# Performance work log

Hardware: AMD Instinct MI355X
Metric: run time of the kernel (lower is better)

The kernel has to match this reference:

```python
import jax, jax.numpy as jnp
import numpy as np

B, L, D, H = 8, 1024, 1024, 16
DK = D // H  # 64
LN_EPS = 1e-5
L2_EPS = 1e-12


def _l2norm(x):
    # torch F.normalize(dim=-1): x / max(||x||_2, eps)
    n = jnp.sqrt(jnp.sum(x * x, axis=-1, keepdims=True))
    return x / jnp.maximum(n, L2_EPS)


def _layernorm(x, gamma, beta):
    mu = jnp.mean(x, axis=-1, keepdims=True)
    var = jnp.mean((x - mu) ** 2, axis=-1, keepdims=True)
    return (x - mu) * jax.lax.rsqrt(var + LN_EPS) * gamma + beta


def setup_inputs() -> dict:
    key = jax.random.key(0)
    ks = jax.random.split(key, 12)
    s = 0.02
    inp = {
        "Q": jax.random.normal(ks[0], (B, L, D), jnp.float32),
        "ctx": jax.random.normal(ks[1], (B, L, D), jnp.float32),
        "attn_mask": jnp.triu(jnp.ones((L, L), bool), 1),  # True = masked (causal)
        # weights stored [in, out] (= torch weight.T) so y = x @ W + b
        "W_q": jax.random.normal(ks[2], (D, D), jnp.float32) * s,
        "b_q": jnp.zeros((D,), jnp.float32),
        "W_k": jax.random.normal(ks[3], (D, D), jnp.float32) * s,
        "b_k": jnp.zeros((D,), jnp.float32),
        "W_v": jax.random.normal(ks[4], (D, D), jnp.float32) * s,
        "b_v": jnp.zeros((D,), jnp.float32),
        "bilinear": jax.random.normal(ks[5], (DK, DK), jnp.float32),
        "ln_gamma": jnp.ones((DK,), jnp.float32),
        "ln_beta": jnp.zeros((DK,), jnp.float32),
        "scale": jnp.asarray(DK ** -0.5, jnp.float32),
        "bias_scale": jnp.asarray(0.1, jnp.float32),
        "W_o": jax.random.normal(ks[6], (D, D), jnp.float32) * s,
        "b_o": jnp.zeros((D,), jnp.float32),
    }
    return inp


def reference(Q, ctx, attn_mask, W_q, b_q, W_k, b_k, W_v, b_v, bilinear,
              ln_gamma, ln_beta, scale, bias_scale, W_o, b_o):
    def split_heads(x):  # [B,L,D] -> [B,H,L,DK]
        return x.reshape(B, L, H, DK).transpose(0, 2, 1, 3)

    q = split_heads(Q @ W_q + b_q)
    k = split_heads(Q @ W_k + b_k)  # self-attention: K = V = Q
    v = split_heads(Q @ W_v + b_v)

    scores = jnp.einsum("bhqd,bhkd->bhqk", q, k) * scale  # [B,H,L,L]
    scores = jnp.where(attn_mask, -jnp.inf, scores)
    attn = jax.nn.softmax(scores, axis=-1)

    # post-softmax bilinear bias: LayerNorm -> bilinear matmul -> L2-normalize
    c = _layernorm(split_heads(ctx), ln_gamma, ln_beta)  # [B,H,L,DK]
    bias = jnp.einsum("bhqe,bhke->bhqk", c @ bilinear, c)  # [B,H,L,L]
    attn = attn + _l2norm(bias) * bias_scale
    attn = _l2norm(attn)

    out = jnp.einsum("bhqk,bhkd->bhqd", attn, v)  # [B,H,L,DK]
    out = out.transpose(0, 2, 1, 3).reshape(B, L, D)
    out = out @ W_o + b_o
    return out
```

## Files before the change

kernel.cpp:

```cpp
#include <hip/hip_runtime.h>


typedef __bf16 bf16;
typedef __bf16 bf16x8 __attribute__((ext_vector_type(8)));
typedef __bf16 bf16x4 __attribute__((ext_vector_type(4)));
typedef float  f32x4  __attribute__((ext_vector_type(4)));

#define DEV static __device__ __forceinline__

DEV f32x4 mfma16(bf16x8 a, bf16x8 b, f32x4 c) {
  return __builtin_amdgcn_mfma_f32_16x16x32_bf16(a, b, c, 0, 0, 0);
}

DEV void async16(void* lds, const void* g) {
  auto* d = reinterpret_cast<__attribute__((address_space(3))) unsigned int*>(
      (unsigned long long)lds);
  auto* s = reinterpret_cast<const __attribute__((address_space(1))) unsigned int*>(
      (unsigned long long)g);
  __builtin_amdgcn_global_load_lds(s, d, 16, 0, 0);
}


__global__ __launch_bounds__(256) void k_cvt(const float* __restrict__ in,
                                             bf16* __restrict__ out, int n4) {
  int i = blockIdx.x * 256 + threadIdx.x;
  if (i >= n4) return;
  f32x4 v = ((const f32x4*)in)[i];
  bf16x4 o = {(bf16)v.x, (bf16)v.y, (bf16)v.z, (bf16)v.w};
  ((bf16x4*)out)[i] = o;
}

__global__ __launch_bounds__(256) void k_transpose_w(const float* __restrict__ in,
                                                     bf16* __restrict__ out) {
  __shared__ float t[64][65];
  const int k0 = blockIdx.x * 64, n0 = blockIdx.y * 64;
  for (int e = threadIdx.x; e < 4096; e += 256) {
    int r = e >> 6, c = e & 63;
    t[r][c] = in[(size_t)(k0 + r) * 1024 + n0 + c];
  }
  __syncthreads();
  for (int e = threadIdx.x; e < 4096; e += 256) {
    int r = e >> 6, c = e & 63;
    out[(size_t)(n0 + r) * 1024 + k0 + c] = (bf16)t[c][r];
  }
}

__global__ __launch_bounds__(256, 4) void k_ln_bilinear(
    const float* __restrict__ ctx, const float* __restrict__ bil,
    const float* __restrict__ gam, const float* __restrict__ bet,
    bf16* __restrict__ c_out, bf16* __restrict__ cb_out) {
  const int w = threadIdx.x >> 6, lane = threadIdx.x & 63;
  float bilreg[64];
#pragma unroll
  for (int e = 0; e < 64; ++e) bilreg[e] = bil[e * 64 + lane];
  const float gm = gam[lane], bt = bet[lane];
  const int wid = blockIdx.x * 4 + w;
  for (int it = 0; it < 16; ++it) {
    const int row = wid * 16 + it;
    const int h = row & 15, bl = row >> 4;
    const float x = ctx[(size_t)row * 64 + lane];
    float s1 = x, s2 = x * x;
#pragma unroll
    for (int mm = 32; mm >= 1; mm >>= 1) {
      s1 += __shfl_xor(s1, mm);
      s2 += __shfl_xor(s2, mm);
    }
    const float mu = s1 * 0.015625f;
    const float var = s2 * 0.015625f - mu * mu;
    const float cv = (x - mu) * rsqrtf(var + 1e-5f) * gm + bt;
    float a0 = 0.f, a1 = 0.f, a2 = 0.f, a3 = 0.f;
#pragma unroll
    for (int e = 0; e < 64; e += 4) {
      a0 += __int_as_float(__builtin_amdgcn_readlane(__float_as_int(cv), e + 0)) * bilreg[e + 0];
      a1 += __int_as_float(__builtin_amdgcn_readlane(__float_as_int(cv), e + 1)) * bilreg[e + 1];
      a2 += __int_as_float(__builtin_amdgcn_readlane(__float_as_int(cv), e + 2)) * bilreg[e + 2];
      a3 += __int_as_float(__builtin_amdgcn_readlane(__float_as_int(cv), e + 3)) * bilreg[e + 3];
    }
    const float acc = (a0 + a1) + (a2 + a3);
    const size_t o =
        ((size_t)((bl >> 10) * 16 + h) * 1024 + (bl & 1023)) * 64 + lane;
    c_out[o] = (bf16)cv;
    cb_out[o] = (bf16)acc;
  }
}


struct GemmPtrs {
  const bf16* Bt[3];
  bf16* ob[3];
  const float* bias[3];
};

__global__ __launch_bounds__(256) void k_gemm(const bf16* __restrict__ A,
                                              GemmPtrs p,
                                              float* __restrict__ outf,
                                              int mode) {
  __shared__ __align__(16) bf16 lds[2][2][4096];
  const int tid = threadIdx.x;
  const int bm = blockIdx.x, bn = blockIdx.y, z = blockIdx.z;
  const int w = tid >> 6, lane = tid & 63, g = lane >> 4, x = lane & 15;
  const int wr = w >> 1, wc = w & 1;
  const bf16* Bt = p.Bt[z];
  const float* bias = p.bias[z];
  bf16* ob = p.ob[z];

  f32x4 acc[4][4];
#pragma unroll
  for (int mt = 0; mt < 4; ++mt)
#pragma unroll
    for (int nt = 0; nt < 4; ++nt) acc[mt][nt] = f32x4{0.f, 0.f, 0.f, 0.f};

  const bf16* Ab = A + (size_t)bm * 128 * 1024;
  const bf16* Bb = Bt + (size_t)bn * 128 * 1024;

  auto stage = [&](int buf, int t) {
#pragma unroll
    for (int i = 0; i < 2; ++i) {
      int ch = i * 256 + tid;
      int r = ch >> 2, s = ch & 3;
      int sg = (s ^ ((r >> 1) & 3)) * 8;
      async16(&lds[buf][0][ch * 8], Ab + (size_t)r * 1024 + t * 32 + sg);
      async16(&lds[buf][1][ch * 8], Bb + (size_t)r * 1024 + t * 32 + sg);
    }
  };

  stage(0, 0);
  const int sa = (g ^ ((x >> 1) & 3)) * 8;
  for (int kt = 0; kt < 32; ++kt) {
    __syncthreads();
    if (kt + 1 < 32) stage((kt + 1) & 1, kt + 1);
    const bf16* la = lds[kt & 1][0];
    const bf16* lb = lds[kt & 1][1];
    bf16x8 af[4], bfr[4];
#pragma unroll
    for (int mt = 0; mt < 4; ++mt)
      af[mt] = *(const bf16x8*)(la + (wr * 64 + mt * 16 + x) * 32 + sa);
#pragma unroll
    for (int nt = 0; nt < 4; ++nt)
      bfr[nt] = *(const bf16x8*)(lb + (wc * 64 + nt * 16 + x) * 32 + sa);
#pragma unroll
    for (int mt = 0; mt < 4; ++mt)
#pragma unroll
      for (int nt = 0; nt < 4; ++nt)
        acc[mt][nt] = mfma16(af[mt], bfr[nt], acc[mt][nt]);
  }

  const int ibase = bm * 128 + wr * 64;
  const int jbase = bn * 128 + wc * 64;
  float bias4[4];
#pragma unroll
  for (int nt = 0; nt < 4; ++nt) bias4[nt] = bias[jbase + nt * 16 + x];

  if (mode < 3) {
    if (z == 2) {
#pragma unroll
      for (int mt = 0; mt < 4; ++mt)
#pragma unroll
        for (int nt = 0; nt < 4; ++nt) {
          const int jj = jbase + nt * 16 + x;
          const int hh = jj >> 6, dk = jj & 63;
          const int i0 = ibase + mt * 16 + 4 * g;
          const int bb = i0 >> 10, l0 = i0 & 1023;
          bf16x4 v4 = {(bf16)(acc[mt][nt][0] + bias4[nt]),
                       (bf16)(acc[mt][nt][1] + bias4[nt]),
                       (bf16)(acc[mt][nt][2] + bias4[nt]),
                       (bf16)(acc[mt][nt][3] + bias4[nt])};
          *(bf16x4*)&ob[((size_t)(bb * 16 + hh) * 64 + dk) * 1024 + l0] = v4;
        }
    } else {
#pragma unroll
      for (int mt = 0; mt < 4; ++mt)
#pragma unroll
        for (int nt = 0; nt < 4; ++nt) {
          const int jj = jbase + nt * 16 + x;
          const int hh = jj >> 6, dk = jj & 63;
#pragma unroll
          for (int j = 0; j < 4; ++j) {
            const int i = ibase + mt * 16 + 4 * g + j;
            const int bb = i >> 10, l = i & 1023;
            ob[(((size_t)bb * 16 + hh) * 1024 + l) * 64 + dk] =
                (bf16)(acc[mt][nt][j] + bias4[nt]);
          }
        }
    }
  } else {
#pragma unroll
    for (int mt = 0; mt < 4; ++mt)
#pragma unroll
      for (int nt = 0; nt < 4; ++nt) {
        const int jj = jbase + nt * 16 + x;
#pragma unroll
        for (int j = 0; j < 4; ++j) {
          const int i = ibase + mt * 16 + 4 * g + j;
          outf[(size_t)i * 1024 + jj] = acc[mt][nt][j] + bias4[nt];
        }
      }
  }
}

__global__ __launch_bounds__(256, 4) void k_attn(
    const bf16* __restrict__ qg, const bf16* __restrict__ kg,
    const bf16* __restrict__ vTg, const bf16* __restrict__ cg,
    const bf16* __restrict__ cbg, bf16* __restrict__ ao,
    const float* __restrict__ scale_p, const float* __restrict__ bsp) {
  __shared__ __align__(16) bf16 kl[2][2048];
  __shared__ __align__(16) bf16 cl[2][2048];
  __shared__ __align__(16) bf16 vl[2][64][36];
  __shared__ __align__(16) bf16 pe[4][640];
  __shared__ __align__(16) bf16 pb[4][640];

  const float scl = scale_p[0];
  const float bsc = bsp[0];
  const int tid = threadIdx.x, w = tid >> 6, lane = tid & 63;
  const int g = lane >> 4, x = lane & 15;
  const int id = blockIdx.x;
  const int xcd = id & 7, sid = id >> 3;
  const int bh = xcd * 16 + (sid >> 4);
  const int qt = sid & 15;
  const int qrow0 = qt * 64 + w * 16;

  const bf16* qrow = qg + ((size_t)bh * 1024 + qrow0 + x) * 64;
  const bf16* cbrow = cbg + ((size_t)bh * 1024 + qrow0 + x) * 64;
  const bf16x8 qf0 = *(const bf16x8*)(qrow + 8 * g);
  const bf16x8 qf1 = *(const bf16x8*)(qrow + 32 + 8 * g);
  const bf16x8 cbf0 = *(const bf16x8*)(cbrow + 8 * g);
  const bf16x8 cbf1 = *(const bf16x8*)(cbrow + 32 + 8 * g);

  f32x4 acc1[4], acc2[4];
#pragma unroll
  for (int i = 0; i < 4; ++i) {
    acc1[i] = f32x4{0.f, 0.f, 0.f, 0.f};
    acc2[i] = f32x4{0.f, 0.f, 0.f, 0.f};
  }
  float Zs = 0.f, E2 = 0.f, Cc = 0.f, B2 = 0.f;

  const bf16* kbh = kg + (size_t)bh * 65536;
  const bf16* cbh = cg + (size_t)bh * 65536;
  const bf16* vbh = vTg + (size_t)bh * 65536;
  const int nK = 2 * qt + 2;

  auto stageKC = [&](int buf, int t) {
    const int r = tid >> 3, s = tid & 7;
    const int sg = (s ^ (r & 7)) * 8;
    if (t < nK)
      async16(&kl[buf][tid * 8], kbh + (size_t)(t * 32 + r) * 64 + sg);
    async16(&cl[buf][tid * 8], cbh + (size_t)(t * 32 + r) * 64 + sg);
  };
  bf16x8 vreg;
  auto loadV = [&](int t) {
    const int r = tid >> 2, s = tid & 3;
    vreg = *(const bf16x8*)(vbh + (size_t)r * 1024 + t * 32 + s * 8);
  };
  auto writeV = [&](int buf) {
    const int r = tid >> 2, s = tid & 3;
    *(bf16x8*)&vl[buf][r][(s ^ (r & 3)) * 8] = vreg;
  };

  stageKC(0, 0);
  loadV(0);
  writeV(0);
  for (int t = 0; t < 32; ++t) {
    __syncthreads();
    if (t + 1 < 32) {
      stageKC((t + 1) & 1, t + 1);
      loadV(t + 1);
    }
    const bf16* klb = kl[t & 1];
    const bf16* clb = cl[t & 1];
    const int tileK = t * 32;
    const bool hv = tileK <= qrow0 + 15;
    float sv[8], bv[8];
#pragma unroll
    for (int sub = 0; sub < 2; ++sub) {
      const int rloc = sub * 16 + x;
      const int so0 = (g ^ (rloc & 7)) * 8;
      const int so1 = ((4 + g) ^ (rloc & 7)) * 8;
      const bf16* cr = clb + rloc * 64;
      f32x4 bacc = f32x4{0.f, 0.f, 0.f, 0.f};
      bacc = mfma16(*(const bf16x8*)(cr + so0), cbf0, bacc);
      bacc = mfma16(*(const bf16x8*)(cr + so1), cbf1, bacc);
      const int k16 = tileK + sub * 16;
      const bool av = k16 <= qrow0 + 15;
      const bool full = (k16 + 15) <= qrow0;
      f32x4 sacc = f32x4{0.f, 0.f, 0.f, 0.f};
      if (av) {
        const bf16* kr = klb + rloc * 64;
        sacc = mfma16(*(const bf16x8*)(kr + so0), qf0, sacc);
        sacc = mfma16(*(const bf16x8*)(kr + so1), qf1, sacc);
      }
      const int q = qrow0 + x;
#pragma unroll
      for (int j = 0; j < 4; ++j) {
        bv[sub * 4 + j] = bacc[j];
        B2 += bacc[j] * bacc[j];
        const int kk = k16 + 4 * g + j;
        sv[sub * 4 + j] =
            full ? sacc[j] * scl
                 : ((av && kk <= q) ? sacc[j] * scl : -1e30f);
      }
    }
    if (hv) {
      float ev[8];
#pragma unroll
      for (int jj = 0; jj < 8; ++jj) {
        const float e = __expf(sv[jj]);
        ev[jj] = e;
        Zs += e; E2 += e * e; Cc += e * bv[jj];
      }
      bf16x4 e0 = {(bf16)ev[0], (bf16)ev[1], (bf16)ev[2], (bf16)ev[3]};
      bf16x4 e1 = {(bf16)ev[4], (bf16)ev[5], (bf16)ev[6], (bf16)ev[7]};
      *(bf16x4*)&pe[w][x * 40 + 4 * g] = e0;
      *(bf16x4*)&pe[w][x * 40 + 16 + 4 * g] = e1;
    }
    bf16x4 b0 = {(bf16)bv[0], (bf16)bv[1], (bf16)bv[2], (bf16)bv[3]};
    bf16x4 b1 = {(bf16)bv[4], (bf16)bv[5], (bf16)bv[6], (bf16)bv[7]};
    *(bf16x4*)&pb[w][x * 40 + 4 * g] = b0;
    *(bf16x4*)&pb[w][x * 40 + 16 + 4 * g] = b1;
    const bf16x8 pbf = *(const bf16x8*)&pb[w][x * 40 + 8 * g];
#pragma unroll
    for (int nt = 0; nt < 4; ++nt) {
      const int dr = nt * 16 + x;
      const bf16x8 vf = *(const bf16x8*)&vl[t & 1][dr][(g ^ (dr & 3)) * 8];
      acc2[nt] = mfma16(pbf, vf, acc2[nt]);
    }
    if (hv) {
      const bf16x8 pef = *(const bf16x8*)&pe[w][x * 40 + 8 * g];
#pragma unroll
      for (int nt = 0; nt < 4; ++nt) {
        const int dr = nt * 16 + x;
        const bf16x8 vf = *(const bf16x8*)&vl[t & 1][dr][(g ^ (dr & 3)) * 8];
        acc1[nt] = mfma16(pef, vf, acc1[nt]);
      }
    }
    if (t + 1 < 32) writeV((t + 1) & 1);
  }

  Zs += __shfl_xor(Zs, 16); Zs += __shfl_xor(Zs, 32);
  E2 += __shfl_xor(E2, 16); E2 += __shfl_xor(E2, 32);
  Cc += __shfl_xor(Cc, 16); Cc += __shfl_xor(Cc, 32);
  B2 += __shfl_xor(B2, 16); B2 += __shfl_xor(B2, 32);
  const float bnorm = fmaxf(sqrtf(B2), 1e-12f);
  const float invZ = 1.0f / Zs;
  const float n2 = E2 * invZ * invZ + 2.0f * bsc * Cc * invZ / bnorm +
                   bsc * bsc * B2 / (bnorm * bnorm);
  const float inv_an = 1.0f / fmaxf(sqrtf(n2), 1e-12f);
  const float cA = invZ * inv_an;
  const float cB = bsc / bnorm * inv_an;
  const int b_ = bh >> 4, h_ = bh & 15;
#pragma unroll
  for (int j = 0; j < 4; ++j) {
    const int src = (lane & 48) | (4 * g + j);
    const float cAj = __shfl(cA, src);
    const float cBj = __shfl(cB, src);
    const int qr = qrow0 + 4 * g + j;
#pragma unroll
    for (int nt = 0; nt < 4; ++nt) {
      const float o = cAj * acc1[nt][j] + cBj * acc2[nt][j];
      ao[(size_t)(b_ * 1024 + qr) * 1024 + h_ * 64 + nt * 16 + x] = (bf16)o;
    }
  }
}


extern "C" void kernel_launch(void* const* d_in, const int* in_sizes, int n_in,
                              void* d_out, int out_size, void* d_ws,
                              size_t ws_size, hipStream_t stream) {
  const float* Q   = (const float*)d_in[0];
  const float* ctx = (const float*)d_in[1];
  const float* Wq  = (const float*)d_in[3];
  const float* bq  = (const float*)d_in[4];
  const float* Wk  = (const float*)d_in[5];
  const float* bk  = (const float*)d_in[6];
  const float* Wv  = (const float*)d_in[7];
  const float* bvp = (const float*)d_in[8];
  const float* bil = (const float*)d_in[9];
  const float* gam = (const float*)d_in[10];
  const float* bet = (const float*)d_in[11];
  const float* scl = (const float*)d_in[12];
  const float* bsc = (const float*)d_in[13];
  const float* Wo  = (const float*)d_in[14];
  const float* bo  = (const float*)d_in[15];
  float* out = (float*)d_out;
  char* ws = (char*)d_ws;
  const size_t MB = 1ull << 20;

  bf16* Qb  = (bf16*)(ws + 0);
  bf16* Wtq = (bf16*)(ws + 16 * MB);
  bf16* Wtk = (bf16*)(ws + 18 * MB);
  bf16* Wtv = (bf16*)(ws + 20 * MB);
  bf16* Wto = (bf16*)(ws + 22 * MB);
  bf16* qb  = (bf16*)(ws + 24 * MB);
  bf16* kb  = (bf16*)(ws + 40 * MB);
  bf16* vT  = (bf16*)(ws + 72 * MB);
  bf16* cN  = (bf16*)(ws + 88 * MB);
  bf16* cbN = (bf16*)(ws + 104 * MB);
  bf16* ao  = Qb;

  k_cvt<<<8192, 256, 0, stream>>>(Q, Qb, 2097152);
  k_transpose_w<<<dim3(16, 16), 256, 0, stream>>>(Wq, Wtq);
  k_transpose_w<<<dim3(16, 16), 256, 0, stream>>>(Wk, Wtk);
  k_transpose_w<<<dim3(16, 16), 256, 0, stream>>>(Wv, Wtv);
  k_transpose_w<<<dim3(16, 16), 256, 0, stream>>>(Wo, Wto);
  k_ln_bilinear<<<2048, 256, 0, stream>>>(ctx, bil, gam, bet, cN, cbN);

  GemmPtrs p1{{Wtq, Wtk, Wtv}, {qb, kb, vT}, {bq, bk, bvp}};
  k_gemm<<<dim3(64, 8, 3), 256, 0, stream>>>(Qb, p1, nullptr, 0);

  k_attn<<<2048, 256, 0, stream>>>(qb, kb, vT, cN, cbN, ao, scl, bsc);

  GemmPtrs p2{{Wto, Wto, Wto}, {nullptr, nullptr, nullptr}, {bo, bo, bo}};
  k_gemm<<<dim3(64, 8, 1), 256, 0, stream>>>(ao, p2, out, 3);

  (void)in_sizes; (void)n_in; (void)out_size; (void)ws_size;
}
```

Baseline: 411.6 us.

## Factor bilinear bias through per-head Gram matrices and skip masked key tiles

The bilinear-bias term over all keys is low-rank, so it is rewritten algebraically. Per-head matrices M = Vᵀ·C and G = Cᵀ·C are precomputed in a new kernel, so the bias contribution to the output and its squared norm become small 64x64 products per query row. The cross term between softmax weights and bias is obtained by accumulating P·C alongside P·V. This lets the attention loop stop at the causal boundary instead of scanning all 1024 keys, roughly halving the work. It costs an extra transpose of C, a small Gram kernel, and some extra bf16 rounding in the norm computation.

Measured after the change: 422.6 us. +2.7%, slower.

```diff
diff --git a/kernel.cpp b/kernel.cpp
--- a/kernel.cpp
+++ b/kernel.cpp
@@ -42,6 +42,23 @@
   for (int e = threadIdx.x; e < 4096; e += 256) {
     int r = e >> 6, c = e & 63;
     out[(size_t)(n0 + r) * 1024 + k0 + c] = (bf16)t[c][r];
+  }
+}
+
+__global__ __launch_bounds__(256) void k_transpose_c(const bf16* __restrict__ in,
+                                                     bf16* __restrict__ out) {
+  __shared__ bf16 t[64][65];
+  const int bh = blockIdx.y, k0 = blockIdx.x * 64;
+  const bf16* src = in + (size_t)bh * 65536;
+  bf16* dst = out + (size_t)bh * 65536;
+  for (int e = threadIdx.x; e < 4096; e += 256) {
+    int r = e >> 6, c = e & 63;
+    t[r][c] = src[(size_t)(k0 + r) * 64 + c];
+  }
+  __syncthreads();
+  for (int e = threadIdx.x; e < 4096; e += 256) {
+    int r = e >> 6, c = e & 63;
+    dst[(size_t)r * 1024 + k0 + c] = t[c][r];
   }
 }
 
@@ -82,6 +99,35 @@
     c_out[o] = (bf16)cv;
     cb_out[o] = (bf16)acc;
   }
+}
+
+__global__ __launch_bounds__(256) void k_mg(const bf16* __restrict__ vT,
+                                            const bf16* __restrict__ cT,
+                                            bf16* __restrict__ mg) {
+  const int which = blockIdx.x, bh = blockIdx.y;
+  const int w = threadIdx.x >> 6, lane = threadIdx.x & 63;
+  const int g = lane >> 4, x = lane & 15;
+  const bf16* A = (which ? cT : vT) + (size_t)bh * 65536;
+  const bf16* Bm = cT + (size_t)bh * 65536;
+  f32x4 acc[4];
+#pragma unroll
+  for (int nt = 0; nt < 4; ++nt) acc[nt] = f32x4{0.f, 0.f, 0.f, 0.f};
+  const bf16* arow = A + (size_t)(w * 16 + x) * 1024 + 8 * g;
+  for (int k = 0; k < 32; ++k) {
+    const bf16x8 af = *(const bf16x8*)(arow + k * 32);
+#pragma unroll
+    for (int nt = 0; nt < 4; ++nt) {
+      const bf16x8 bf = *(const bf16x8*)(Bm + (size_t)(nt * 16 + x) * 1024 +
+                                         k * 32 + 8 * g);
+      acc[nt] = mfma16(af, bf, acc[nt]);
+    }
+  }
+  bf16* out = mg + (size_t)bh * 8192 + which * 4096;
+#pragma unroll
+  for (int nt = 0; nt < 4; ++nt)
+#pragma unroll
+    for (int j = 0; j < 4; ++j)
+      out[(w * 16 + 4 * g + j) * 64 + nt * 16 + x] = (bf16)acc[nt][j];
 }
 
 
@@ -200,14 +246,14 @@
 
 __global__ __launch_bounds__(256, 4) void k_attn(
     const bf16* __restrict__ qg, const bf16* __restrict__ kg,
-    const bf16* __restrict__ vTg, const bf16* __restrict__ cg,
-    const bf16* __restrict__ cbg, bf16* __restrict__ ao,
+    const bf16* __restrict__ vTg, const bf16* __restrict__ cTg,
+    const bf16* __restrict__ cbg, const bf16* __restrict__ mg,
+    bf16* __restrict__ ao,
     const float* __restrict__ scale_p, const float* __restrict__ bsp) {
   __shared__ __align__(16) bf16 kl[2][2048];
-  __shared__ __align__(16) bf16 cl[2][2048];
+  __shared__ __align__(16) bf16 ctl[2][64][36];
   __shared__ __align__(16) bf16 vl[2][64][36];
   __shared__ __align__(16) bf16 pe[4][640];
-  __shared__ __align__(16) bf16 pb[4][640];
 
   const float scl = scale_p[0];
   const float bsc = bsp[0];
@@ -226,136 +272,175 @@
   const bf16x8 cbf0 = *(const bf16x8*)(cbrow + 8 * g);
   const bf16x8 cbf1 = *(const bf16x8*)(cbrow + 32 + 8 * g);
 
-  f32x4 acc1[4], acc2[4];
+  f32x4 acc1[4], acc3[4];
 #pragma unroll
   for (int i = 0; i < 4; ++i) {
     acc1[i] = f32x4{0.f, 0.f, 0.f, 0.f};
-    acc2[i] = f32x4{0.f, 0.f, 0.f, 0.f};
-  }
-  float Zs = 0.f, E2 = 0.f, Cc = 0.f, B2 = 0.f;
+    acc3[i] = f32x4{0.f, 0.f, 0.f, 0.f};
+  }
+  float Zs = 0.f, E2 = 0.f;
 
   const bf16* kbh = kg + (size_t)bh * 65536;
-  const bf16* cbh = cg + (size_t)bh * 65536;
+  const bf16* ctbh = cTg + (size_t)bh * 65536;
   const bf16* vbh = vTg + (size_t)bh * 65536;
   const int nK = 2 * qt + 2;
 
-  auto stageKC = [&](int buf, int t) {
+  auto stageK = [&](int buf, int t) {
     const int r = tid >> 3, s = tid & 7;
     const int sg = (s ^ (r & 7)) * 8;
-    if (t < nK)
-      async16(&kl[buf][tid * 8], kbh + (size_t)(t * 32 + r) * 64 + sg);
-    async16(&cl[buf][tid * 8], cbh + (size_t)(t * 32 + r) * 64 + sg);
+    async16(&kl[buf][tid * 8], kbh + (size_t)(t * 32 + r) * 64 + sg);
   };
-  bf16x8 vreg;
-  auto loadV = [&](int t) {
+  bf16x8 vreg, creg;
+  auto loadCV = [&](int t) {
     const int r = tid >> 2, s = tid & 3;
     vreg = *(const bf16x8*)(vbh + (size_t)r * 1024 + t * 32 + s * 8);
+    creg = *(const bf16x8*)(ctbh + (size_t)r * 1024 + t * 32 + s * 8);
   };
-  auto writeV = [&](int buf) {
+  auto writeCV = [&](int buf) {
     const int r = tid >> 2, s = tid & 3;
     *(bf16x8*)&vl[buf][r][(s ^ (r & 3)) * 8] = vreg;
+    *(bf16x8*)&ctl[buf][r][(s ^ (r & 3)) * 8] = creg;
   };
 
-  stageKC(0, 0);
-  loadV(0);
-  writeV(0);
-  for (int t = 0; t < 32; ++t) {
+  stageK(0, 0);
+  loadCV(0);
+  writeCV(0);
+  for (int t = 0; t < nK; ++t) {
     __syncthreads();
-    if (t + 1 < 32) {
-      stageKC((t + 1) & 1, t + 1);
-      loadV(t + 1);
+    if (t + 1 < nK) {
+      stageK((t + 1) & 1, t + 1);
+      loadCV(t + 1);
     }
     const bf16* klb = kl[t & 1];
-    const bf16* clb = cl[t & 1];
     const int tileK = t * 32;
     const bool hv = tileK <= qrow0 + 15;
-    float sv[8], bv[8];
-#pragma unroll
-    for (int sub = 0; sub < 2; ++sub) {
-      const int rloc = sub * 16 + x;
-      const int so0 = (g ^ (rloc & 7)) * 8;
-      const int so1 = ((4 + g) ^ (rloc & 7)) * 8;
-      const bf16* cr = clb + rloc * 64;
-      f32x4 bacc = f32x4{0.f, 0.f, 0.f, 0.f};
-      bacc = mfma16(*(const bf16x8*)(cr + so0), cbf0, bacc);
-      bacc = mfma16(*(const bf16x8*)(cr + so1), cbf1, bacc);
-      const int k16 = tileK + sub * 16;
-      const bool av = k16 <= qrow0 + 15;
-      const bool full = (k16 + 15) <= qrow0;
-      f32x4 sacc = f32x4{0.f, 0.f, 0.f, 0.f};
-      if (av) {
-        const bf16* kr = klb + rloc * 64;
-        sacc = mfma16(*(const bf16x8*)(kr + so0), qf0, sacc);
-        sacc = mfma16(*(const bf16x8*)(kr + so1), qf1, sacc);
+    if (hv) {
+      float sv[8];
+#pragma unroll
+      for (int sub = 0; sub < 2; ++sub) {
+        const int rloc = sub * 16 + x;
+        const int so0 = (g ^ (rloc & 7)) * 8;
+        const int so1 = ((4 + g) ^ (rloc & 7)) * 8;
+        const int k16 = tileK + sub * 16;
+        const bool av = k16 <= qrow0 + 15;
+        const bool full = (k16 + 15) <= qrow0;
+        f32x4 sacc = f32x4{0.f, 0.f, 0.f, 0.f};
+        if (av) {
+          const bf16* kr = klb + rloc * 64;
+          sacc = mfma16(*(const bf16x8*)(kr + so0), qf0, sacc);
+          sacc = mfma16(*(const bf16x8*)(kr + so1), qf1, sacc);
+        }
+        const int q = qrow0 + x;
+#pragma unroll
+        for (int j = 0; j < 4; ++j) {
+          const int kk = k16 + 4 * g + j;
+          sv[sub * 4 + j] =
+              full ? sacc[j] * scl
+                   : ((av && kk <= q) ? sacc[j] * scl : -1e30f);
+        }
       }
-      const int q = qrow0 + x;
-#pragma unroll
-      for (int j = 0; j < 4; ++j) {
-        bv[sub * 4 + j] = bacc[j];
-        B2 += bacc[j] * bacc[j];
-        const int kk = k16 + 4 * g + j;
-        sv[sub * 4 + j] =
-            full ? sacc[j] * scl
-                 : ((av && kk <= q) ? sacc[j] * scl : -1e30f);
-      }
-    }
-    if (hv) {
       float ev[8];
 #pragma unroll
       for (int jj = 0; jj < 8; ++jj) {
         const float e = __expf(sv[jj]);
         ev[jj] = e;
-        Zs += e; E2 += e * e; Cc += e * bv[jj];
+        Zs += e; E2 += e * e;
       }
       bf16x4 e0 = {(bf16)ev[0], (bf16)ev[1], (bf16)ev[2], (bf16)ev[3]};
       bf16x4 e1 = {(bf16)ev[4], (bf16)ev[5], (bf16)ev[6], (bf16)ev[7]};
       *(bf16x4*)&pe[w][x * 40 + 4 * g] = e0;
       *(bf16x4*)&pe[w][x * 40 + 16 + 4 * g] = e1;
-    }
-    bf16x4 b0 = {(bf16)bv[0], (bf16)bv[1], (bf16)bv[2], (bf16)bv[3]};
-    bf16x4 b1 = {(bf16)bv[4], (bf16)bv[5], (bf16)bv[6], (bf16)bv[7]};
-    *(bf16x4*)&pb[w][x * 40 + 4 * g] = b0;
-    *(bf16x4*)&pb[w][x * 40 + 16 + 4 * g] = b1;
-    const bf16x8 pbf = *(const bf16x8*)&pb[w][x * 40 + 8 * g];
-#pragma unroll
-    for (int nt = 0; nt < 4; ++nt) {
-      const int dr = nt * 16 + x;
-      const bf16x8 vf = *(const bf16x8*)&vl[t & 1][dr][(g ^ (dr & 3)) * 8];
-      acc2[nt] = mfma16(pbf, vf, acc2[nt]);
-    }
-    if (hv) {
       const bf16x8 pef = *(const bf16x8*)&pe[w][x * 40 + 8 * g];
 #pragma unroll
       for (int nt = 0; nt < 4; ++nt) {
         const int dr = nt * 16 + x;
-        const bf16x8 vf = *(const bf16x8*)&vl[t & 1][dr][(g ^ (dr & 3)) * 8];
+        const int ch = (g ^ (dr & 3)) * 8;
+        const bf16x8 vf = *(const bf16x8*)&vl[t & 1][dr][ch];
+        const bf16x8 cf = *(const bf16x8*)&ctl[t & 1][dr][ch];
         acc1[nt] = mfma16(pef, vf, acc1[nt]);
+        acc3[nt] = mfma16(pef, cf, acc3[nt]);
       }
     }
-    if (t + 1 < 32) writeV((t + 1) & 1);
+    if (t + 1 < nK) writeCV((t + 1) & 1);
   }
 
   Zs += __shfl_xor(Zs, 16); Zs += __shfl_xor(Zs, 32);
   E2 += __shfl_xor(E2, 16); E2 += __shfl_xor(E2, 32);
-  Cc += __shfl_xor(Cc, 16); Cc += __shfl_xor(Cc, 32);
-  B2 += __shfl_xor(B2, 16); B2 += __shfl_xor(B2, 32);
-  const float bnorm = fmaxf(sqrtf(B2), 1e-12f);
+
+  float cbv[4][4];
+#pragma unroll
+  for (int nt = 0; nt < 4; ++nt)
+#pragma unroll
+    for (int j = 0; j < 4; ++j)
+      cbv[nt][j] = (float)cbg[((size_t)bh * 1024 + qrow0 + 4 * g + j) * 64 +
+                              nt * 16 + x];
+
+  float cc4[4] = {0.f, 0.f, 0.f, 0.f};
+#pragma unroll
+  for (int nt = 0; nt < 4; ++nt)
+#pragma unroll
+    for (int j = 0; j < 4; ++j) cc4[j] += acc3[nt][j] * cbv[nt][j];
+#pragma unroll
+  for (int j = 0; j < 4; ++j) {
+    cc4[j] += __shfl_xor(cc4[j], 1);
+    cc4[j] += __shfl_xor(cc4[j], 2);
+    cc4[j] += __shfl_xor(cc4[j], 4);
+    cc4[j] += __shfl_xor(cc4[j], 8);
+  }
+  const bf16* Gm = mg + (size_t)bh * 8192 + 4096;
+  float b24[4] = {0.f, 0.f, 0.f, 0.f};
+#pragma unroll
+  for (int nt = 0; nt < 4; ++nt) {
+    const bf16* grow = Gm + (nt * 16 + x) * 64;
+    f32x4 uu = f32x4{0.f, 0.f, 0.f, 0.f};
+    uu = mfma16(cbf0, *(const bf16x8*)(grow + 8 * g), uu);
+    uu = mfma16(cbf1, *(const bf16x8*)(grow + 32 + 8 * g), uu);
+#pragma unroll
+    for (int j = 0; j < 4; ++j) b24[j] += uu[j] * cbv[nt][j];
+  }
+#pragma unroll
+  for (int j = 0; j < 4; ++j) {
+    b24[j] += __shfl_xor(b24[j], 1);
+    b24[j] += __shfl_xor(b24[j], 2);
+    b24[j] += __shfl_xor(b24[j], 4);
+    b24[j] += __shfl_xor(b24[j], 8);
+  }
+  const int jsel = lane & 3;
+  const float ccsel = jsel == 0 ? cc4[0] : jsel == 1 ? cc4[1]
+                     : jsel == 2 ? cc4[2] : cc4[3];
+  const float b2sel = jsel == 0 ? b24[0] : jsel == 1 ? b24[1]
+                     : jsel == 2 ? b24[2] : b24[3];
+  const int src = ((x >> 2) << 4) | (x & 3);
+  const float CcX = __shfl(ccsel, src);
+  const float B2X = fmaxf(__shfl(b2sel, src), 0.f);
+
+  const bf16* Mm = mg + (size_t)bh * 8192;
+  f32x4 a2[4];
+#pragma unroll
+  for (int nt = 0; nt < 4; ++nt) {
+    const bf16* mrow = Mm + (nt * 16 + x) * 64;
+    a2[nt] = f32x4{0.f, 0.f, 0.f, 0.f};
+    a2[nt] = mfma16(cbf0, *(const bf16x8*)(mrow + 8 * g), a2[nt]);
+    a2[nt] = mfma16(cbf1, *(const bf16x8*)(mrow + 32 + 8 * g), a2[nt]);
+  }
+
+  const float bnorm = fmaxf(sqrtf(B2X), 1e-12f);
   const float invZ = 1.0f / Zs;
-  const float n2 = E2 * invZ * invZ + 2.0f * bsc * Cc * invZ / bnorm +
-                   bsc * bsc * B2 / (bnorm * bnorm);
+  const float n2 = E2 * invZ * invZ + 2.0f * bsc * CcX * invZ / bnorm +
+                   bsc * bsc;
   const float inv_an = 1.0f / fmaxf(sqrtf(n2), 1e-12f);
   const float cA = invZ * inv_an;
   const float cB = bsc / bnorm * inv_an;
   const int b_ = bh >> 4, h_ = bh & 15;
 #pragma unroll
   for (int j = 0; j < 4; ++j) {
-    const int src = (lane & 48) | (4 * g + j);
-    const float cAj = __shfl(cA, src);
-    const float cBj = __shfl(cB, src);
+    const int srcq = (lane & 48) | (4 * g + j);
+    const float cAj = __shfl(cA, srcq);
+    const float cBj = __shfl(cB, srcq);
     const int qr = qrow0 + 4 * g + j;
 #pragma unroll
     for (int nt = 0; nt < 4; ++nt) {
-      const float o = cAj * acc1[nt][j] + cBj * acc2[nt][j];
+      const float o = cAj * acc1[nt][j] + cBj * a2[nt][j];
       ao[(size_t)(b_ * 1024 + qr) * 1024 + h_ * 64 + nt * 16 + x] = (bf16)o;
     }
   }
@@ -391,9 +476,11 @@
   bf16* Wto = (bf16*)(ws + 22 * MB);
   bf16* qb  = (bf16*)(ws + 24 * MB);
   bf16* kb  = (bf16*)(ws + 40 * MB);
+  bf16* cT  = (bf16*)(ws + 56 * MB);
   bf16* vT  = (bf16*)(ws + 72 * MB);
   bf16* cN  = (bf16*)(ws + 88 * MB);
   bf16* cbN = (bf16*)(ws + 104 * MB);
+  bf16* mg  = Wtq;
   bf16* ao  = Qb;
 
   k_cvt<<<8192, 256, 0, stream>>>(Q, Qb, 2097152);
@@ -402,11 +489,13 @@
   k_transpose_w<<<dim3(16, 16), 256, 0, stream>>>(Wv, Wtv);
   k_transpose_w<<<dim3(16, 16), 256, 0, stream>>>(Wo, Wto);
   k_ln_bilinear<<<2048, 256, 0, stream>>>(ctx, bil, gam, bet, cN, cbN);
+  k_transpose_c<<<dim3(16, 128), 256, 0, stream>>>(cN, cT);
 
   GemmPtrs p1{{Wtq, Wtk, Wtv}, {qb, kb, vT}, {bq, bk, bvp}};
   k_gemm<<<dim3(64, 8, 3), 256, 0, stream>>>(Qb, p1, nullptr, 0);
 
-  k_attn<<<2048, 256, 0, stream>>>(qb, kb, vT, cN, cbN, ao, scl, bsc);
+  k_mg<<<dim3(2, 128), 256, 0, stream>>>(vT, cT, mg);
+  k_attn<<<2048, 256, 0, stream>>>(qb, kb, vT, cT, cbN, mg, ao, scl, bsc);
 
   GemmPtrs p2{{Wto, Wto, Wto}, {nullptr, nullptr, nullptr}, {bo, bo, bo}};
   k_gemm<<<dim3(64, 8, 1), 256, 0, stream>>>(ao, p2, out, 3);
```
